# Optimization experiments

Hardware: AMD Instinct MI355X
Metric: run time of the kernel (lower is better)

The kernel has to match this reference:

```python
import jax, jax.numpy as jnp
import numpy as np

B, S, D_MODEL, H = 2, 2048, 2048, 16
DQK = D_MODEL // H            # 128
DV = D_MODEL * 2 // H // 3    # 85 (GLU branch)
SCALE = DQK ** -0.5
ROPE_BASE = 10000.0


def apply_rope(x):
    # x: [B, S, H, D], NeoX-style half rotation
    D = x.shape[-1]
    half = D // 2
    inv_freq = 1.0 / (ROPE_BASE ** (jnp.arange(half, dtype=jnp.float32) / half))
    ang = jnp.arange(x.shape[1], dtype=jnp.float32)[:, None] * inv_freq[None, :]  # [S, half]
    cos = jnp.cos(ang)[None, :, None, :]
    sin = jnp.sin(ang)[None, :, None, :]
    x1, x2 = x[..., :half], x[..., half:]
    return jnp.concatenate([x1 * cos - x2 * sin, x2 * cos + x1 * sin], axis=-1)


def setup_inputs() -> dict:
    key = jax.random.key(0)
    ks = jax.random.split(key, 12)
    init = lambda k, shape, fan_in: jax.random.uniform(k, shape, jnp.float32, -1.0, 1.0) * (fan_in ** -0.5)
    q = jax.random.normal(ks[0], (B, S, D_MODEL), jnp.float32)
    k = jax.random.normal(ks[1], (B, S, D_MODEL), jnp.float32)
    v = jax.random.normal(ks[2], (B, S, D_MODEL), jnp.float32)
    # causal boolean mask: True = masked (upper triangle)
    mask = jnp.triu(jnp.ones((S, S), dtype=bool), k=1)
    Wq = init(ks[3], (D_MODEL, DQK * H), D_MODEL)
    bq = init(ks[4], (DQK * H,), D_MODEL)
    Wk = init(ks[5], (D_MODEL, DQK * H), D_MODEL)
    bk = init(ks[6], (DQK * H,), D_MODEL)
    Wv = init(ks[7], (D_MODEL, DV * H * 2), D_MODEL)
    bv = init(ks[8], (DV * H * 2,), D_MODEL)
    Wo = init(ks[9], (DV * H, D_MODEL), DV * H)
    bo = init(ks[10], (D_MODEL,), DV * H)
    return {"q": q, "k": k, "v": v, "mask": mask,
            "Wq": Wq, "bq": bq, "Wk": Wk, "bk": bk,
            "Wv": Wv, "bv": bv, "Wo": Wo, "bo": bo}


def reference(q, k, v, mask, Wq, bq, Wk, bk, Wv, bv, Wo, bo):
    qp = q @ Wq + bq                      # [B,S,H*DQK]
    kp = k @ Wk + bk                      # [B,S,H*DQK]
    vp = v @ Wv + bv                      # [B,S,2*H*DV]
    # GLU over the FULL last dim (matches torch chunk(2, dim=-1) before unflatten)
    half = DV * H
    vg = vp[..., :half] * jax.nn.silu(vp[..., half:])   # [B,S,H*DV]
    qh = qp.reshape(B, S, H, DQK)
    kh = kp.reshape(B, S, H, DQK)
    vh = vg.reshape(B, S, H, DV)
    qh = apply_rope(qh)
    kh = apply_rope(kh)
    # [B,H,S,D]
    qh = qh.transpose(0, 2, 1, 3)
    kh = kh.transpose(0, 2, 1, 3)
    vh = vh.transpose(0, 2, 1, 3)
    score = jnp.einsum('bhqd,bhkd->bhqk', qh, kh) * SCALE  # [B,H,S,S]
    score = jnp.where(mask[None, None, :, :], -jnp.inf, score)
    attn = jax.nn.softmax(score, axis=-1)
    o = jnp.einsum('bhqk,bhkd->bhqd', attn, vh)            # [B,H,S,DV]
    o = o.transpose(0, 2, 1, 3).reshape(B, S, H * DV)
    return o @ Wo + bo                                     # [B,S,D_MODEL]
```

## Files before the change

kernel.cpp:

```cpp
#include <hip/hip_runtime.h>
#include <cstdint>
#include <cmath>

typedef __bf16 bf16;
typedef __bf16 bf16x8 __attribute__((ext_vector_type(8)));
typedef float f32x4 __attribute__((ext_vector_type(4)));

#define B_      2
#define S_      2048
#define H_      16
#define DQK_    128
#define DV_     85
#define DVP_    96
#define DMODEL_ 2048
#define NKV_    1360
#define KH_     1536
#define NV_     2720
#define NVP_    2816
#define SCALE_  0.08838834764831845f
#define QSCALE_ 0.12752044442215615f
#define M2_     16.0f
#define L2_10K_ 13.287712379549449f

__device__ __forceinline__ void lds_cp16(const void* g, void* l) {
    __builtin_amdgcn_global_load_lds(
        (const __attribute__((address_space(1))) unsigned int*)(uintptr_t)g,
        (__attribute__((address_space(3))) unsigned int*)(uintptr_t)l,
        16, 0, 0);
}

__global__ __launch_bounds__(256) void detect_dtype(const unsigned int* __restrict__ w,
                                                    int* __restrict__ flag) {
    __shared__ int cnt;
    if (threadIdx.x == 0) cnt = 0;
    __syncthreads();
    unsigned v = w[threadIdx.x];
    unsigned e = (v >> 7) & 0xFFu;
    if (e > 100u && e < 140u) atomicAdd(&cnt, 1);
    __syncthreads();
    if (threadIdx.x == 0) *flag = (cnt >= 200) ? 1 : 0;
}

__global__ __launch_bounds__(256) void norm_mat(const void* __restrict__ src, bf16* __restrict__ dst,
                                                const int* __restrict__ flag, long n8) {
    long i = (long)blockIdx.x * 256 + threadIdx.x;
    if (i >= n8) return;
    if (*flag) {
        ((bf16x8*)dst)[i] = ((const bf16x8*)src)[i];
    } else {
        const float* s = (const float*)src;
        bf16x8 v;
#pragma unroll
        for (int j = 0; j < 8; ++j) v[j] = (bf16)s[i * 8 + j];
        ((bf16x8*)dst)[i] = v;
    }
}

__global__ __launch_bounds__(256) void norm_bias4(
    const void* __restrict__ s0, const void* __restrict__ s1,
    const void* __restrict__ s2, const void* __restrict__ s3,
    float* __restrict__ d0, float* __restrict__ d1,
    float* __restrict__ d2, float* __restrict__ d3,
    const int* __restrict__ flag) {
    int j = blockIdx.x * 256 + threadIdx.x;
    const void* s; float* d;
    if (j < DMODEL_) { s = s0; d = d0; }
    else if ((j -= DMODEL_) < DMODEL_) { s = s1; d = d1; }
    else if ((j -= DMODEL_) < NV_) { s = s2; d = d2; }
    else if ((j -= NV_) < DMODEL_) { s = s3; d = d3; }
    else return;
    d[j] = (*flag) ? (float)((const bf16*)s)[j] : ((const float*)s)[j];
}

__global__ __launch_bounds__(256) void transpose_qk_dyn(
    const void* __restrict__ inq, const void* __restrict__ ink,
    bf16* __restrict__ outq, bf16* __restrict__ outk, const int* __restrict__ flag) {
    __shared__ bf16 tile[32][33];
    const bool isbf = (*flag != 0);
    const void* in = blockIdx.z ? ink : inq;
    bf16* out = blockIdx.z ? outk : outq;
    int r0 = blockIdx.x * 32, c0 = blockIdx.y * 32;
    int tx = threadIdx.x, ty = threadIdx.y;
#pragma unroll
    for (int i = 0; i < 32; i += 8) {
        size_t idx = (size_t)(r0 + ty + i) * DMODEL_ + c0 + tx;
        tile[ty + i][tx] = isbf ? ((const bf16*)in)[idx] : (bf16)((const float*)in)[idx];
    }
    __syncthreads();
#pragma unroll
    for (int i = 0; i < 32; i += 8)
        out[(size_t)(c0 + ty + i) * DMODEL_ + r0 + tx] = tile[tx][ty + i];
}

__global__ __launch_bounds__(256) void transpose_wvi_dyn(
    const void* __restrict__ in, bf16* __restrict__ out, const int* __restrict__ flag) {
    __shared__ bf16 tile[32][34];
    const bool isbf = (*flag != 0);
    int n0 = blockIdx.x * 32, k0 = blockIdx.y * 32;
    int tx = threadIdx.x, ty = threadIdx.y;
    int fl = (n0 >> 1) + (tx & 15), vg = tx >> 4;
    int c = vg * NKV_ + fl;
    int nl = 2 * (tx & 15) + vg;
#pragma unroll
    for (int i = 0; i < 32; i += 8) {
        bf16 v = (bf16)0.0f;
        if (fl < NKV_) {
            size_t idx = (size_t)(k0 + ty + i) * NV_ + c;
            v = isbf ? ((const bf16*)in)[idx] : (bf16)((const float*)in)[idx];
        }
        tile[ty + i][nl] = v;
    }
    __syncthreads();
#pragma unroll
    for (int i = 0; i < 32; i += 8)
        out[(size_t)(n0 + ty + i) * DMODEL_ + k0 + tx] = tile[tx][ty + i];
}

__global__ __launch_bounds__(256) void transpose_wo_dyn(
    const void* __restrict__ in, bf16* __restrict__ out, const int* __restrict__ flag) {
    __shared__ bf16 tile[32][33];
    const bool isbf = (*flag != 0);
    int k0 = blockIdx.x * 32, n0 = blockIdx.y * 32;
    int tx = threadIdx.x, ty = threadIdx.y;
#pragma unroll
    for (int i = 0; i < 32; i += 8) {
        int k = k0 + ty + i, c = n0 + tx;
        int hh = k / DVP_, dd = k - hh * DVP_;
        bf16 v = (bf16)0.0f;
        if (dd < DV_) {
            size_t idx = (size_t)(hh * DV_ + dd) * DMODEL_ + c;
            v = isbf ? ((const bf16*)in)[idx] : (bf16)((const float*)in)[idx];
        }
        tile[ty + i][tx] = v;
    }
    __syncthreads();
#pragma unroll
    for (int i = 0; i < 32; i += 8) {
        int n = n0 + ty + i, k = k0 + tx;
        out[(size_t)n * KH_ + k] = tile[tx][ty + i];
    }
}

__global__ __launch_bounds__(256) void gemm_qk_rope(
    const bf16* __restrict__ Aq, const bf16* __restrict__ Ak,
    const bf16* __restrict__ Btq, const bf16* __restrict__ Btk,
    const float* __restrict__ bq, const float* __restrict__ bk,
    bf16* __restrict__ qt, bf16* __restrict__ ktp) {
    __shared__ bf16 As[128 * 32];
    __shared__ bf16 Bs[128 * 32];
    __shared__ bf16 ep[64 * 132];
    const int z = blockIdx.z;
    const bf16* A    = z ? Ak  : Aq;
    const bf16* Bt   = z ? Btk : Btq;
    const float* bias = z ? bk : bq;
    bf16* dst        = z ? ktp : qt;
    const float qs   = z ? 1.0f : QSCALE_;
    const int t = threadIdx.x, lane = t & 63, w = t >> 6;
    const int m0 = blockIdx.x * 128, n0 = blockIdx.y * 128;
    const int wm = (w >> 1) * 64, wn = (w & 1) * 64;
    const int fm = lane & 15, quad = lane >> 4, fk = quad * 8;
    const int srow = lane >> 2, scol = (lane & 3) * 8;
    f32x4 acc[4][4] = {};
    for (int k0 = 0; k0 < DMODEL_; k0 += 32) {
        __syncthreads();
#pragma unroll
        for (int j = 0; j < 2; ++j) {
            int c = j * 4 + w;
            lds_cp16(A + (size_t)(m0 + c * 16 + srow) * DMODEL_ + k0 + scol, &As[c * 512]);
            lds_cp16(Bt + (size_t)(n0 + c * 16 + srow) * DMODEL_ + k0 + scol, &Bs[c * 512]);
        }
        __syncthreads();
        bf16x8 af[4], bfr[4];
#pragma unroll
        for (int i = 0; i < 4; ++i) {
            af[i]  = *(const bf16x8*)&As[(wm + i * 16 + fm) * 32 + fk];
            bfr[i] = *(const bf16x8*)&Bs[(wn + i * 16 + fm) * 32 + fk];
        }
#pragma unroll
        for (int i = 0; i < 4; ++i)
#pragma unroll
            for (int jn = 0; jn < 4; ++jn)
                acc[i][jn] = __builtin_amdgcn_mfma_f32_16x16x32_bf16(af[i], bfr[jn], acc[i][jn], 0, 0, 0);
    }
    const int h = blockIdx.y;
    const int b = m0 >> 11, s_base = m0 & (S_ - 1);
    float bv[4];
#pragma unroll
    for (int jn = 0; jn < 4; ++jn) bv[jn] = bias[n0 + wn + jn * 16 + fm];
    bf16* dbase = dst + (size_t)(b * H_ + h) * S_ * DQK_;
#pragma unroll
    for (int ph = 0; ph < 2; ++ph) {
        if ((w >> 1) == ph) {
#pragma unroll
            for (int i = 0; i < 4; ++i)
#pragma unroll
                for (int jn = 0; jn < 4; ++jn)
#pragma unroll
                    for (int r = 0; r < 4; ++r)
                        ep[(i * 16 + quad * 4 + r) * 132 + wn + jn * 16 + fm] =
                            (bf16)(acc[i][jn][r] + bv[jn]);
        }
        __syncthreads();
#pragma unroll
        for (int it2 = 0; it2 < 4; ++it2) {
            int task = it2 * 256 + t;
            int lr = task >> 4, ch = task & 15;
            int s = s_base + ph * 64 + lr;
            bf16x8 v = *(const bf16x8*)&ep[lr * 132 + ch * 8];
            bf16x8 u = *(const bf16x8*)&ep[lr * 132 + ((ch * 8) ^ 64)];
            bf16x8 o8;
#pragma unroll
            for (int j = 0; j < 8; ++j) {
                int d = ch * 8 + j, dd = d & 63;
                float ang = (float)s * exp2f(-(float)dd * (L2_10K_ / 64.0f));
                float sn, cs;
                __sincosf(ang, &sn, &cs);
                float x = (float)v[j], y = (float)u[j];
                float ov = (d < 64) ? (x * cs - y * sn) : (x * cs + y * sn);
                o8[j] = (bf16)(ov * qs);
            }
            *(bf16x8*)&dbase[(size_t)s * DQK_ + ch * 8] = o8;
        }
        __syncthreads();
    }
}

__global__ __launch_bounds__(256) void gemm_v_swiglu(
    const bf16* __restrict__ A, const bf16* __restrict__ Bt,
    const float* __restrict__ bias, bf16* __restrict__ vt) {
    __shared__ bf16 As[128 * 32];
    __shared__ bf16 Bs[128 * 32];
    __shared__ bf16 ep2[64 * 136];
    const int t = threadIdx.x, lane = t & 63, w = t >> 6;
    const int m0 = blockIdx.x * 128, n0 = blockIdx.y * 128;
    const int wm = (w >> 1) * 64, wn = (w & 1) * 64;
    const int fm = lane & 15, quad = lane >> 4, fk = quad * 8;
    const int srow = lane >> 2, scol = (lane & 3) * 8;
    f32x4 acc[4][4] = {};
    for (int k0 = 0; k0 < DMODEL_; k0 += 32) {
        __syncthreads();
#pragma unroll
        for (int j = 0; j < 2; ++j) {
            int c = j * 4 + w;
            lds_cp16(A + (size_t)(m0 + c * 16 + srow) * DMODEL_ + k0 + scol, &As[c * 512]);
            lds_cp16(Bt + (size_t)(n0 + c * 16 + srow) * DMODEL_ + k0 + scol, &Bs[c * 512]);
        }
        __syncthreads();
        bf16x8 af[4], bfr[4];
#pragma unroll
        for (int i = 0; i < 4; ++i) {
            af[i]  = *(const bf16x8*)&As[(wm + i * 16 + fm) * 32 + fk];
            bfr[i] = *(const bf16x8*)&Bs[(wn + i * 16 + fm) * 32 + fk];
        }
#pragma unroll
        for (int i = 0; i < 4; ++i)
#pragma unroll
            for (int jn = 0; jn < 4; ++jn)
                acc[i][jn] = __builtin_amdgcn_mfma_f32_16x16x32_bf16(af[i], bfr[jn], acc[i][jn], 0, 0, 0);
    }
    float bv[4];
#pragma unroll
    for (int jn = 0; jn < 4; ++jn) {
        int col = n0 + wn + jn * 16 + fm;
        bv[jn] = (col < NV_) ? bias[(col & 1) * NKV_ + (col >> 1)] : 0.0f;
    }
    const bool isval = ((fm & 1) == 0);
    const int fl_base = (wn >> 1) + (fm >> 1);
    const int s_base = wm + quad * 4;
#pragma unroll
    for (int i = 0; i < 4; ++i)
#pragma unroll
        for (int jn = 0; jn < 4; ++jn)
#pragma unroll
            for (int r = 0; r < 4; ++r) {
                float ag = acc[i][jn][r] + bv[jn];
                float part = __shfl_xor(ag, 1, 64);
                if (isval) {
                    float g = part;
                    float out = ag * g / (1.0f + __expf(-g));
                    ep2[(fl_base + jn * 8) * 136 + s_base + i * 16 + r] = (bf16)out;
                }
            }
    __syncthreads();
    const int b = m0 >> 11, s0 = m0 & (S_ - 1);
#pragma unroll
    for (int it2 = 0; it2 < 4; ++it2) {
        int task = it2 * 256 + t;
        int fl_local = task >> 4, ch = task & 15;
        int flat = blockIdx.y * 64 + fl_local;
        if (flat < NKV_) {
            int h = (flat * 1543) >> 17;
            int d = flat - h * DV_;
            bf16x8 v = *(const bf16x8*)&ep2[fl_local * 136 + ch * 8];
            *(bf16x8*)&vt[((size_t)(b * H_ + h) * DVP_ + d) * S_ + s0 + ch * 8] = v;
        }
    }
}

__global__ __launch_bounds__(256) void vt_pad(bf16* __restrict__ vt) {
    int idx = blockIdx.x * 256 + threadIdx.x;
    if (idx >= 32 * 11 * 2048) return;
    int s = idx & (S_ - 1);
    int rest = idx >> 11;
    int dpad = 85 + rest % 11;
    int bh = rest / 11;
    vt[((size_t)bh * DVP_ + dpad) * S_ + s] = (bf16)((dpad == 95) ? 1.0f : 0.0f);
}

__global__ __launch_bounds__(256) void gemm_bt_oh(
    const bf16* __restrict__ Oh, const bf16* __restrict__ Bt,
    const float* __restrict__ bias, bf16* __restrict__ C, float* __restrict__ Cf,
    const int* __restrict__ outflag) {
    __shared__ bf16 As[128 * 32];
    __shared__ bf16 Bs[128 * 32];
    const int t = threadIdx.x, lane = t & 63, w = t >> 6;
    const int m0 = blockIdx.x * 128, n0 = blockIdx.y * 128;
    const int wm = (w >> 1) * 64, wn = (w & 1) * 64;
    const int fm = lane & 15, quad = lane >> 4, fk = quad * 8;
    const int srow = lane >> 2, scol = (lane & 3) * 8;
    f32x4 acc[4][4] = {};
    for (int k0 = 0; k0 < KH_; k0 += 32) {
        __syncthreads();
#pragma unroll
        for (int j = 0; j < 2; ++j) {
            int c = j * 4 + w;
            int m = m0 + c * 16 + srow;
            int k = k0 + scol;
            int hh = k / DVP_, dd = k - hh * DVP_;
            const bf16* ga = Oh + ((size_t)((m >> 11) * H_ + hh) * S_ + (m & (S_ - 1))) * DVP_ + dd;
            lds_cp16(ga, &As[c * 512]);
            lds_cp16(Bt + (size_t)(n0 + c * 16 + srow) * KH_ + k0 + scol, &Bs[c * 512]);
        }
        __syncthreads();
        bf16x8 af[4], bfr[4];
#pragma unroll
        for (int i = 0; i < 4; ++i) {
            af[i]  = *(const bf16x8*)&As[(wm + i * 16 + fm) * 32 + fk];
            bfr[i] = *(const bf16x8*)&Bs[(wn + i * 16 + fm) * 32 + fk];
        }
#pragma unroll
        for (int i = 0; i < 4; ++i)
#pragma unroll
            for (int jn = 0; jn < 4; ++jn)
                acc[i][jn] = __builtin_amdgcn_mfma_f32_16x16x32_bf16(af[i], bfr[jn], acc[i][jn], 0, 0, 0);
    }
    bool bf16out = (*outflag != 0);
#pragma unroll
    for (int jn = 0; jn < 4; ++jn) {
        int col = n0 + wn + jn * 16 + fm;
        float bv = bias[col];
#pragma unroll
        for (int i = 0; i < 4; ++i) {
            int rowb = m0 + wm + i * 16 + quad * 4;
            if (bf16out) {
#pragma unroll
                for (int r = 0; r < 4; ++r)
                    C[(size_t)(rowb + r) * DMODEL_ + col] = (bf16)(acc[i][jn][r] + bv);
            } else {
#pragma unroll
                for (int r = 0; r < 4; ++r)
                    Cf[(size_t)(rowb + r) * DMODEL_ + col] = acc[i][jn][r] + bv;
            }
        }
    }
}

__global__ __launch_bounds__(256) void attn_split(
    const bf16* __restrict__ qt, const bf16* __restrict__ kt,
    const bf16* __restrict__ vt,
    bf16* __restrict__ Opart, float* __restrict__ lpart) {
    const int bh = blockIdx.x, qb = blockIdx.y, split = blockIdx.z;
    if (split * 8 > qb) return;
    __shared__ bf16 Ks[64 * 128];
    __shared__ bf16 Vs[96 * 64];
    __shared__ bf16 plds[4][16 * 72];
    const int t = threadIdx.x, lane = t & 63, w = t >> 6;
    const int fm = lane & 15, quad = lane >> 4;
    const int h = bh & 15, b = bh >> 4;
    const int q0 = qb * 64 + w * 16;
    const int g = qb >> 3;
    const int pidx = bh * 80 + 4 * g * (g + 1) + (qb & 7) * (g + 1) + split;

    const bf16* qbase = qt + ((size_t)(b * H_ + h) * S_ + q0 + fm) * DQK_ + quad * 8;
    bf16x8 aq[4];
#pragma unroll
    for (int kb = 0; kb < 4; ++kb) aq[kb] = *(const bf16x8*)(qbase + kb * 32);
    const bf16* kbase = kt + (size_t)(b * H_ + h) * S_ * DQK_;
    const bf16* vbase = vt + (size_t)(b * H_ + h) * DVP_ * S_;

    const float NEG_INF = -__builtin_inff();
    f32x4 oacc[6] = {};
    bf16* pl = &plds[w][0];

    const int t0 = split * 8;
    const int t1 = min(t0 + 8, qb + 1);
    for (int it = t0; it < t1; ++it) {
        const int k0 = it * 64;
        __syncthreads();
#pragma unroll
        for (int iw = 0; iw < 4; ++iw) {
            int flat = (w * 4 + iw) * 64 + lane;
            int r = flat >> 4, c = (flat & 15) ^ (r & 15);
            lds_cp16(kbase + (size_t)(k0 + r) * DQK_ + c * 8, &Ks[(w * 4 + iw) * 512]);
        }
#pragma unroll
        for (int iw = 0; iw < 3; ++iw) {
            int flat = (w * 3 + iw) * 64 + lane;
            int r = flat >> 3, c = (flat & 7) ^ (r & 7);
            lds_cp16(vbase + (size_t)r * S_ + k0 + c * 8, &Vs[(w * 3 + iw) * 512]);
        }
        __syncthreads();
        f32x4 sc[4] = {};
#pragma unroll
        for (int nt = 0; nt < 4; ++nt) {
            if (k0 + nt * 16 <= q0 + 15) {
                const int row16 = (nt * 16 + fm) * 16;
#pragma unroll
                for (int kb = 0; kb < 4; ++kb) {
                    const bf16* kp = &Ks[(row16 + ((kb * 4 + quad) ^ fm)) * 8];
                    sc[nt] = __builtin_amdgcn_mfma_f32_16x16x32_bf16(aq[kb], *(const bf16x8*)kp, sc[nt], 0, 0, 0);
                }
            }
        }
        if (it == qb) {
#pragma unroll
            for (int nt = 0; nt < 4; ++nt) {
                int col = k0 + nt * 16 + fm;
#pragma unroll
                for (int r = 0; r < 4; ++r) {
                    int rowq = q0 + quad * 4 + r;
                    if (col > rowq) sc[nt][r] = NEG_INF;
                }
            }
        }
#pragma unroll
        for (int nt = 0; nt < 4; ++nt)
#pragma unroll
            for (int r = 0; r < 4; ++r)
                pl[(quad * 4 + r) * 72 + nt * 16 + fm] =
                    (bf16)__builtin_amdgcn_exp2f(sc[nt][r] - M2_);
        asm volatile("s_waitcnt lgkmcnt(0)" ::: "memory");
        bf16x8 pa0 = *(const bf16x8*)(pl + fm * 72 + quad * 8);
        bf16x8 pa1 = *(const bf16x8*)(pl + fm * 72 + 32 + quad * 8);
#pragma unroll
        for (int n2 = 0; n2 < 6; ++n2) {
            int row8 = (n2 * 16 + fm) * 8;
            const bf16* v0 = &Vs[(row8 + (quad ^ (fm & 7))) * 8];
            const bf16* v1 = &Vs[(row8 + ((4 + quad) ^ (fm & 7))) * 8];
            oacc[n2] = __builtin_amdgcn_mfma_f32_16x16x32_bf16(pa0, *(const bf16x8*)v0, oacc[n2], 0, 0, 0);
            oacc[n2] = __builtin_amdgcn_mfma_f32_16x16x32_bf16(pa1, *(const bf16x8*)v1, oacc[n2], 0, 0, 0);
        }
    }
    float lv[4], inv_l[4];
#pragma unroll
    for (int r = 0; r < 4; ++r) {
        lv[r] = __shfl(oacc[5][r], (lane & 48) | 15, 64);
        inv_l[r] = (lv[r] > 0.f) ? 1.0f / lv[r] : 0.0f;
    }
    if (fm == 0) {
#pragma unroll
        for (int r = 0; r < 4; ++r) {
            int row = w * 16 + quad * 4 + r;
            lpart[(size_t)pidx * 64 + row] = lv[r];
        }
    }
#pragma unroll
    for (int n2 = 0; n2 < 6; ++n2)
#pragma unroll
        for (int r = 0; r < 4; ++r) {
            int row = w * 16 + quad * 4 + r;
            Opart[((size_t)pidx * 64 + row) * DVP_ + n2 * 16 + fm] = (bf16)(oacc[n2][r] * inv_l[r]);
        }
}

__global__ __launch_bounds__(256) void attn_combine2(
    const bf16* __restrict__ Opart, const float* __restrict__ lpart,
    bf16* __restrict__ oh) {
    const int bh = blockIdx.x, qb = blockIdx.y;
    const int g = qb >> 3, nact = g + 1;
    const int pidx0 = bh * 80 + 4 * g * (g + 1) + (qb & 7) * (g + 1);
    const int t = threadIdx.x;
#pragma unroll
    for (int i = 0; i < 3; ++i) {
        int idx = i * 256 + t;
        int row = idx / 12, ch = idx - row * 12;
        float W = 0.f, wgt[4];
        for (int p = 0; p < nact; ++p) {
            wgt[p] = lpart[(size_t)(pidx0 + p) * 64 + row];
            W += wgt[p];
        }
        float invW = (W > 0.f) ? 1.0f / W : 0.0f;
        float acc[8] = {};
        for (int p = 0; p < nact; ++p) {
            bf16x8 v = *(const bf16x8*)&Opart[((size_t)(pidx0 + p) * 64 + row) * DVP_ + ch * 8];
#pragma unroll
            for (int j = 0; j < 8; ++j) acc[j] += wgt[p] * (float)v[j];
        }
        bf16x8 o8;
#pragma unroll
        for (int j = 0; j < 8; ++j) o8[j] = (bf16)(acc[j] * invW);
        *(bf16x8*)&oh[((size_t)bh * S_ + qb * 64 + row) * DVP_ + ch * 8] = o8;
    }
}

extern "C" void kernel_launch(void* const* d_in, const int* in_sizes, int n_in,
                              void* d_out, int out_size, void* d_ws, size_t ws_size,
                              hipStream_t stream) {
    const void* qin = d_in[0];
    const void* kin = d_in[1];
    const void* vin = d_in[2];
    const void* Wq = d_in[4];
    const void* bq = d_in[5];
    const void* Wk = d_in[6];
    const void* bk = d_in[7];
    const void* Wv = d_in[8];
    const void* bv = d_in[9];
    const void* Wo = d_in[10];
    const void* bo = d_in[11];

    char* ws = (char*)d_ws;
    bf16* qt   = (bf16*)(ws);
    bf16* ktp  = (bf16*)(ws + 16777216);
    char* R1   = ws + 33554432;
    bf16* scrq = (bf16*)(R1);
    bf16* scrk = (bf16*)(R1 + 16777216);
    bf16* wTq  = (bf16*)(R1 + 33554432);
    bf16* wTk  = (bf16*)(R1 + 41943040);
    bf16* scrv = (bf16*)(R1);
    bf16* wTvi = (bf16*)(R1 + 16777216);
    bf16*  wTo   = (bf16*)(R1);
    bf16*  Opart = (bf16*)(R1 + 6291456);
    float* lpart = (float*)(R1 + 37748736);
    bf16* vtp = (bf16*)(ws + 84148224);
    bf16* oh  = (bf16*)(ws + 96731136);
    float* bqf = (float*)(ws + 109314048);
    float* bkf = bqf + DMODEL_;
    float* bvf = bkf + DMODEL_;
    float* bof = bvf + NV_;
    int*  flag = (int*)(bof + DMODEL_);

    dim3 tb(32, 8);
    auto nblk = [](long n8) { return (int)((n8 + 255) / 256); };
    long n8_x = (long)B_ * S_ * DMODEL_ / 8;

    detect_dtype<<<1, 256, 0, stream>>>((const unsigned int*)qin, flag);
    norm_bias4<<<(3 * DMODEL_ + NV_ + 255) / 256, 256, 0, stream>>>(
        bq, bk, bv, bo, bqf, bkf, bvf, bof, flag);
    vt_pad<<<(32 * 11 * 2048) / 256, 256, 0, stream>>>(vtp);

    norm_mat<<<nblk(n8_x), 256, 0, stream>>>(qin, scrq, flag, n8_x);
    norm_mat<<<nblk(n8_x), 256, 0, stream>>>(kin, scrk, flag, n8_x);
    transpose_qk_dyn<<<dim3(64, 64, 2), tb, 0, stream>>>(Wq, Wk, wTq, wTk, flag);
    gemm_qk_rope<<<dim3(32, 16, 2), 256, 0, stream>>>(scrq, scrk, wTq, wTk, bqf, bkf, qt, ktp);

    norm_mat<<<nblk(n8_x), 256, 0, stream>>>(vin, scrv, flag, n8_x);
    transpose_wvi_dyn<<<dim3(NVP_ / 32, DMODEL_ / 32), tb, 0, stream>>>(Wv, wTvi, flag);
    gemm_v_swiglu<<<dim3(32, NVP_ / 128), 256, 0, stream>>>(scrv, wTvi, bvf, vtp);

    transpose_wo_dyn<<<dim3(KH_ / 32, DMODEL_ / 32), tb, 0, stream>>>(Wo, wTo, flag);

    attn_split<<<dim3(32, 32, 4), 256, 0, stream>>>(qt, ktp, vtp, Opart, lpart);
    attn_combine2<<<dim3(32, 32), 256, 0, stream>>>(Opart, lpart, oh);

    gemm_bt_oh<<<dim3(32, 16), 256, 0, stream>>>(oh, wTo, bof, (bf16*)d_out, (float*)d_out, flag);
}
```

Baseline: 510.1 us.

## Replace QK and V projection GEMMs with 256x256-tile pipelined kernels

Both input-projection GEMMs move from 128x128 tiles on 256 threads to 256x256 tiles on 512 threads. They now share a loop with a 4-slot LDS ring buffer that prefetches the next K slices while MFMAs run, using explicit waitcnt, barriers and raised wave priority around the MFMA block. The aim is more data reuse per LDS load and hiding global-load latency behind compute. In exchange, 128KB of dynamic shared memory limits each CU to one block. The larger tiles also give fewer blocks (256 for QK, 176 for V), which may leave some CUs idle.

```diff
diff --git a/kernel.cpp b/kernel.cpp
--- a/kernel.cpp
+++ b/kernel.cpp
@@ -141,134 +141,179 @@
     }
 }
 
-__global__ __launch_bounds__(256) void gemm_qk_rope(
+template <int NT, class AF>
+__device__ __forceinline__ void gemm256_loop(
+    AF aaddr, const bf16* __restrict__ Bt, int ldb, int n0,
+    bf16* sA, bf16* sB, f32x4 (&acc)[8][4])
+{
+    const int tid = threadIdx.x, lane = tid & 63, w = tid >> 6;
+    const int fm = lane & 15, quad = lane >> 4;
+    const int wm = (w >> 2) * 128, wn = (w & 3) * 64;
+    const int row0 = tid >> 2, kk8 = (tid & 3) * 8;
+
+    auto stageA = [&](int u) {
+        const int ri = u & 3, c = u * 32 + kk8;
+        lds_cp16(aaddr(row0, c),       &sA[ri * 8192 + w * 512]);
+        lds_cp16(aaddr(row0 + 128, c), &sA[ri * 8192 + 4096 + w * 512]);
+    };
+    auto stageB = [&](int u) {
+        const int ri = u & 3, c = u * 32 + kk8;
+        lds_cp16(Bt + (size_t)(n0 + row0) * ldb + c,       &sB[ri * 8192 + w * 512]);
+        lds_cp16(Bt + (size_t)(n0 + row0 + 128) * ldb + c, &sB[ri * 8192 + 4096 + w * 512]);
+    };
+
+    stageA(0); stageB(0); stageA(1); stageB(1);
+    asm volatile("s_waitcnt vmcnt(4)" ::: "memory");
+    __builtin_amdgcn_sched_barrier(0);
+    __builtin_amdgcn_s_barrier();
+    __builtin_amdgcn_sched_barrier(0);
+
+    for (int t = 0; t < NT; ++t) {
+        const int u0 = 2 * t;
+        const bool pre = (t + 1 < NT);
+        bf16x8 af[8], bfv[2];
+#pragma unroll
+        for (int p = 0; p < 4; ++p) {
+            const int kh = p >> 1, nh = p & 1;
+            const int ri = (u0 + kh) & 3;
+            if (nh == 0) {
+#pragma unroll
+                for (int i = 0; i < 8; ++i)
+                    af[i] = *(const bf16x8*)&sA[ri * 8192 + (wm + i * 16 + fm) * 32 + quad * 8];
+            }
+#pragma unroll
+            for (int j = 0; j < 2; ++j)
+                bfv[j] = *(const bf16x8*)&sB[ri * 8192 + (wn + nh * 32 + j * 16 + fm) * 32 + quad * 8];
+            if (pre) {
+                if      (p == 0) stageA(u0 + 2);
+                else if (p == 1) stageB(u0 + 2);
+                else if (p == 2) stageA(u0 + 3);
+                else             stageB(u0 + 3);
+            }
+            __builtin_amdgcn_sched_barrier(0);
+            __builtin_amdgcn_s_barrier();
+            asm volatile("s_waitcnt lgkmcnt(0)" ::: "memory");
+            __builtin_amdgcn_sched_barrier(0);
+            __builtin_amdgcn_s_setprio(1);
+#pragma unroll
+            for (int i = 0; i < 8; ++i)
+#pragma unroll
+                for (int j = 0; j < 2; ++j)
+                    acc[i][nh * 2 + j] = __builtin_amdgcn_mfma_f32_16x16x32_bf16(
+                        af[i], bfv[j], acc[i][nh * 2 + j], 0, 0, 0);
+            __builtin_amdgcn_s_setprio(0);
+            __builtin_amdgcn_sched_barrier(0);
+            if (nh == 1) {
+                if (pre) asm volatile("s_waitcnt vmcnt(4)" ::: "memory");
+                else     asm volatile("s_waitcnt vmcnt(0)" ::: "memory");
+                __builtin_amdgcn_sched_barrier(0);
+            }
+            __builtin_amdgcn_s_barrier();
+            __builtin_amdgcn_sched_barrier(0);
+        }
+    }
+}
+
+__global__ __launch_bounds__(512, 2) void gemm_qk_rope256(
     const bf16* __restrict__ Aq, const bf16* __restrict__ Ak,
     const bf16* __restrict__ Btq, const bf16* __restrict__ Btk,
     const float* __restrict__ bq, const float* __restrict__ bk,
     bf16* __restrict__ qt, bf16* __restrict__ ktp) {
-    __shared__ bf16 As[128 * 32];
-    __shared__ bf16 Bs[128 * 32];
-    __shared__ bf16 ep[64 * 132];
+    extern __shared__ char smem[];
+    bf16* sA = (bf16*)smem;
+    bf16* sB = (bf16*)(smem + 65536);
     const int z = blockIdx.z;
-    const bf16* A    = z ? Ak  : Aq;
-    const bf16* Bt   = z ? Btk : Btq;
-    const float* bias = z ? bk : bq;
-    bf16* dst        = z ? ktp : qt;
-    const float qs   = z ? 1.0f : QSCALE_;
-    const int t = threadIdx.x, lane = t & 63, w = t >> 6;
-    const int m0 = blockIdx.x * 128, n0 = blockIdx.y * 128;
-    const int wm = (w >> 1) * 64, wn = (w & 1) * 64;
-    const int fm = lane & 15, quad = lane >> 4, fk = quad * 8;
-    const int srow = lane >> 2, scol = (lane & 3) * 8;
-    f32x4 acc[4][4] = {};
-    for (int k0 = 0; k0 < DMODEL_; k0 += 32) {
+    const bf16* A     = z ? Ak  : Aq;
+    const bf16* Bt    = z ? Btk : Btq;
+    const float* bias = z ? bk  : bq;
+    bf16* dst         = z ? ktp : qt;
+    const float qs    = z ? 1.0f : QSCALE_;
+    const int tid = threadIdx.x, lane = tid & 63, w = tid >> 6;
+    const int fm = lane & 15, quad = lane >> 4;
+    const int wm = (w >> 2) * 128, wn = (w & 3) * 64;
+    const int m0 = blockIdx.x * 256, n0 = blockIdx.y * 256;
+    f32x4 acc[8][4] = {};
+    auto aaddr = [&](int row, int k) -> const bf16* {
+        return A + (size_t)(m0 + row) * DMODEL_ + k;
+    };
+    gemm256_loop<32>(aaddr, Bt, DMODEL_, n0, sA, sB, acc);
+
+    float bv[4];
+#pragma unroll
+    for (int jn = 0; jn < 4; ++jn) bv[jn] = bias[n0 + wn + jn * 16 + fm];
+    const int b = m0 >> 11, sb = m0 & (S_ - 1);
+    const int hbase = n0 >> 7;
+    bf16* ep = (bf16*)smem;
+    __syncthreads();
+#pragma unroll
+    for (int g = 0; g < 4; ++g) {
+        if ((w >> 2) == (g >> 1)) {
+#pragma unroll
+            for (int i2 = 0; i2 < 4; ++i2) {
+                const int i = (g & 1) * 4 + i2;
+#pragma unroll
+                for (int jn = 0; jn < 4; ++jn)
+#pragma unroll
+                    for (int r = 0; r < 4; ++r)
+                        ep[(i2 * 16 + quad * 4 + r) * 264 + wn + jn * 16 + fm] =
+                            (bf16)(acc[i][jn][r] + bv[jn]);
+            }
+        }
         __syncthreads();
 #pragma unroll
-        for (int j = 0; j < 2; ++j) {
-            int c = j * 4 + w;
-            lds_cp16(A + (size_t)(m0 + c * 16 + srow) * DMODEL_ + k0 + scol, &As[c * 512]);
-            lds_cp16(Bt + (size_t)(n0 + c * 16 + srow) * DMODEL_ + k0 + scol, &Bs[c * 512]);
-        }
-        __syncthreads();
-        bf16x8 af[4], bfr[4];
-#pragma unroll
-        for (int i = 0; i < 4; ++i) {
-            af[i]  = *(const bf16x8*)&As[(wm + i * 16 + fm) * 32 + fk];
-            bfr[i] = *(const bf16x8*)&Bs[(wn + i * 16 + fm) * 32 + fk];
-        }
-#pragma unroll
-        for (int i = 0; i < 4; ++i)
-#pragma unroll
-            for (int jn = 0; jn < 4; ++jn)
-                acc[i][jn] = __builtin_amdgcn_mfma_f32_16x16x32_bf16(af[i], bfr[jn], acc[i][jn], 0, 0, 0);
-    }
-    const int h = blockIdx.y;
-    const int b = m0 >> 11, s_base = m0 & (S_ - 1);
-    float bv[4];
-#pragma unroll
-    for (int jn = 0; jn < 4; ++jn) bv[jn] = bias[n0 + wn + jn * 16 + fm];
-    bf16* dbase = dst + (size_t)(b * H_ + h) * S_ * DQK_;
-#pragma unroll
-    for (int ph = 0; ph < 2; ++ph) {
-        if ((w >> 1) == ph) {
-#pragma unroll
-            for (int i = 0; i < 4; ++i)
-#pragma unroll
-                for (int jn = 0; jn < 4; ++jn)
-#pragma unroll
-                    for (int r = 0; r < 4; ++r)
-                        ep[(i * 16 + quad * 4 + r) * 132 + wn + jn * 16 + fm] =
-                            (bf16)(acc[i][jn][r] + bv[jn]);
-        }
-        __syncthreads();
-#pragma unroll
         for (int it2 = 0; it2 < 4; ++it2) {
-            int task = it2 * 256 + t;
-            int lr = task >> 4, ch = task & 15;
-            int s = s_base + ph * 64 + lr;
-            bf16x8 v = *(const bf16x8*)&ep[lr * 132 + ch * 8];
-            bf16x8 u = *(const bf16x8*)&ep[lr * 132 + ((ch * 8) ^ 64)];
+            int task = it2 * 512 + tid;
+            int lr = task >> 5, ch = task & 31;
+            int s = sb + g * 64 + lr;
+            int h = hbase + (ch >> 4);
+            int cl0 = (ch * 8) & 127;
+            bf16x8 v  = *(const bf16x8*)&ep[lr * 264 + ch * 8];
+            bf16x8 uu = *(const bf16x8*)&ep[lr * 264 + ((ch * 8) ^ 64)];
             bf16x8 o8;
 #pragma unroll
             for (int j = 0; j < 8; ++j) {
-                int d = ch * 8 + j, dd = d & 63;
+                int cl = cl0 + j, dd = cl & 63;
                 float ang = (float)s * exp2f(-(float)dd * (L2_10K_ / 64.0f));
                 float sn, cs;
                 __sincosf(ang, &sn, &cs);
-                float x = (float)v[j], y = (float)u[j];
-                float ov = (d < 64) ? (x * cs - y * sn) : (x * cs + y * sn);
+                float x = (float)v[j], y = (float)uu[j];
+                float ov = (cl < 64) ? (x * cs - y * sn) : (x * cs + y * sn);
                 o8[j] = (bf16)(ov * qs);
             }
-            *(bf16x8*)&dbase[(size_t)s * DQK_ + ch * 8] = o8;
+            *(bf16x8*)&dst[((size_t)(b * H_ + h) * S_ + s) * DQK_ + cl0] = o8;
         }
         __syncthreads();
     }
 }
 
-__global__ __launch_bounds__(256) void gemm_v_swiglu(
+__global__ __launch_bounds__(512, 2) void gemm_v_swiglu256(
     const bf16* __restrict__ A, const bf16* __restrict__ Bt,
     const float* __restrict__ bias, bf16* __restrict__ vt) {
-    __shared__ bf16 As[128 * 32];
-    __shared__ bf16 Bs[128 * 32];
-    __shared__ bf16 ep2[64 * 136];
-    const int t = threadIdx.x, lane = t & 63, w = t >> 6;
-    const int m0 = blockIdx.x * 128, n0 = blockIdx.y * 128;
-    const int wm = (w >> 1) * 64, wn = (w & 1) * 64;
-    const int fm = lane & 15, quad = lane >> 4, fk = quad * 8;
-    const int srow = lane >> 2, scol = (lane & 3) * 8;
-    f32x4 acc[4][4] = {};
-    for (int k0 = 0; k0 < DMODEL_; k0 += 32) {
-        __syncthreads();
-#pragma unroll
-        for (int j = 0; j < 2; ++j) {
-            int c = j * 4 + w;
-            lds_cp16(A + (size_t)(m0 + c * 16 + srow) * DMODEL_ + k0 + scol, &As[c * 512]);
-            lds_cp16(Bt + (size_t)(n0 + c * 16 + srow) * DMODEL_ + k0 + scol, &Bs[c * 512]);
-        }
-        __syncthreads();
-        bf16x8 af[4], bfr[4];
-#pragma unroll
-        for (int i = 0; i < 4; ++i) {
-            af[i]  = *(const bf16x8*)&As[(wm + i * 16 + fm) * 32 + fk];
-            bfr[i] = *(const bf16x8*)&Bs[(wn + i * 16 + fm) * 32 + fk];
-        }
-#pragma unroll
-        for (int i = 0; i < 4; ++i)
-#pragma unroll
-            for (int jn = 0; jn < 4; ++jn)
-                acc[i][jn] = __builtin_amdgcn_mfma_f32_16x16x32_bf16(af[i], bfr[jn], acc[i][jn], 0, 0, 0);
-    }
+    extern __shared__ char smem[];
+    bf16* sA = (bf16*)smem;
+    bf16* sB = (bf16*)(smem + 65536);
+    const int tid = threadIdx.x, lane = tid & 63, w = tid >> 6;
+    const int fm = lane & 15, quad = lane >> 4;
+    const int wm = (w >> 2) * 128, wn = (w & 3) * 64;
+    const int m0 = blockIdx.x * 256, n0 = blockIdx.y * 256;
+    f32x4 acc[8][4] = {};
+    auto aaddr = [&](int row, int k) -> const bf16* {
+        return A + (size_t)(m0 + row) * DMODEL_ + k;
+    };
+    gemm256_loop<32>(aaddr, Bt, DMODEL_, n0, sA, sB, acc);
+
     float bv[4];
 #pragma unroll
     for (int jn = 0; jn < 4; ++jn) {
         int col = n0 + wn + jn * 16 + fm;
         bv[jn] = (col < NV_) ? bias[(col & 1) * NKV_ + (col >> 1)] : 0.0f;
     }
+    bf16* ep2 = (bf16*)smem;
+    __syncthreads();
     const bool isval = ((fm & 1) == 0);
-    const int fl_base = (wn >> 1) + (fm >> 1);
-    const int s_base = wm + quad * 4;
-#pragma unroll
-    for (int i = 0; i < 4; ++i)
+    const int flb = (wn >> 1) + (fm >> 1);
+#pragma unroll
+    for (int i = 0; i < 8; ++i)
 #pragma unroll
         for (int jn = 0; jn < 4; ++jn)
 #pragma unroll
@@ -276,23 +321,23 @@
                 float ag = acc[i][jn][r] + bv[jn];
                 float part = __shfl_xor(ag, 1, 64);
                 if (isval) {
-                    float g = part;
-                    float out = ag * g / (1.0f + __expf(-g));
-                    ep2[(fl_base + jn * 8) * 136 + s_base + i * 16 + r] = (bf16)out;
+                    float gg = part;
+                    float out = ag * gg / (1.0f + __expf(-gg));
+                    ep2[(flb + jn * 8) * 264 + wm + i * 16 + quad * 4 + r] = (bf16)out;
                 }
             }
     __syncthreads();
     const int b = m0 >> 11, s0 = m0 & (S_ - 1);
 #pragma unroll
-    for (int it2 = 0; it2 < 4; ++it2) {
-        int task = it2 * 256 + t;
-        int fl_local = task >> 4, ch = task & 15;
-        int flat = blockIdx.y * 64 + fl_local;
+    for (int it2 = 0; it2 < 8; ++it2) {
+        int task = it2 * 512 + tid;
+        int fl_local = task >> 5, ch = task & 31;
+        int flat = blockIdx.y * 128 + fl_local;
         if (flat < NKV_) {
             int h = (flat * 1543) >> 17;
             int d = flat - h * DV_;
-            bf16x8 v = *(const bf16x8*)&ep2[fl_local * 136 + ch * 8];
-            *(bf16x8*)&vt[((size_t)(b * H_ + h) * DVP_ + d) * S_ + s0 + ch * 8] = v;
+            bf16x8 vv = *(const bf16x8*)&ep2[fl_local * 264 + ch * 8];
+            *(bf16x8*)&vt[((size_t)(b * H_ + h) * DVP_ + d) * S_ + s0 + ch * 8] = vv;
         }
     }
 }
@@ -543,6 +588,15 @@
     auto nblk = [](long n8) { return (int)((n8 + 255) / 256); };
     long n8_x = (long)B_ * S_ * DMODEL_ / 8;
 
+    static bool attr_done = false;
+    if (!attr_done) {
+        hipFuncSetAttribute((const void*)gemm_qk_rope256,
+                            hipFuncAttributeMaxDynamicSharedMemorySize, 131072);
+        hipFuncSetAttribute((const void*)gemm_v_swiglu256,
+                            hipFuncAttributeMaxDynamicSharedMemorySize, 131072);
+        attr_done = true;
+    }
+
     detect_dtype<<<1, 256, 0, stream>>>((const unsigned int*)qin, flag);
     norm_bias4<<<(3 * DMODEL_ + NV_ + 255) / 256, 256, 0, stream>>>(
         bq, bk, bv, bo, bqf, bkf, bvf, bof, flag);
@@ -551,11 +605,12 @@
     norm_mat<<<nblk(n8_x), 256, 0, stream>>>(qin, scrq, flag, n8_x);
     norm_mat<<<nblk(n8_x), 256, 0, stream>>>(kin, scrk, flag, n8_x);
     transpose_qk_dyn<<<dim3(64, 64, 2), tb, 0, stream>>>(Wq, Wk, wTq, wTk, flag);
-    gemm_qk_rope<<<dim3(32, 16, 2), 256, 0, stream>>>(scrq, scrk, wTq, wTk, bqf, bkf, qt, ktp);
+    gemm_qk_rope256<<<dim3(16, 8, 2), 512, 131072, stream>>>(
+        scrq, scrk, wTq, wTk, bqf, bkf, qt, ktp);
 
     norm_mat<<<nblk(n8_x), 256, 0, stream>>>(vin, scrv, flag, n8_x);
     transpose_wvi_dyn<<<dim3(NVP_ / 32, DMODEL_ / 32), tb, 0, stream>>>(Wv, wTvi, flag);
-    gemm_v_swiglu<<<dim3(32, NVP_ / 128), 256, 0, stream>>>(scrv, wTvi, bvf, vtp);
+    gemm_v_swiglu256<<<dim3(16, NVP_ / 256), 512, 131072, stream>>>(scrv, wTvi, bvf, vtp);
 
     transpose_wo_dyn<<<dim3(KH_ / 32, DMODEL_ / 32), tb, 0, stream>>>(Wo, wTo, flag);
 
```

Result: faster. 496.1 us (-2.7%).
